# Optimization experiments

Hardware: AMD Instinct MI355X
Metric: run time of the kernel (lower is better)

The kernel has to match this reference:

```python
import jax, jax.numpy as jnp
import numpy as np

B, N, DV = 32, 1024, 512
L, S, DT = 256, 8, 512
VOCAB = 1024
BAND = 16
LN_EPS = 1e-5


def setup_inputs() -> dict:
    key = jax.random.key(0)
    ks = jax.random.split(key, 12)
    w = lambda k, shp: jax.random.normal(k, shp, dtype=jnp.float32) * 0.02
    return {
        "vis_tokens": jax.random.normal(ks[0], (B, N, DV), dtype=jnp.float32),
        "txt_ctx_ids": jax.random.randint(ks[1], (B, L, S), 0, VOCAB, dtype=jnp.int32),
        "emb_w": w(ks[2], (VOCAB, DT)),        # embedding table, tied with classifier
        "wq": w(ks[3], (DV, DT)),              # q_proj: d_txt -> d_vis
        "wk": w(ks[4], (DV, DV)),
        "wv": w(ks[5], (DV, DV)),
        "wv2t": w(ks[6], (DT, DV)),            # vis2txt: d_vis -> d_txt
        "dw_k": w(ks[7], (DT, 1, 3)),          # depthwise conv1d kernel (O, I/g=1, K)
        "pw_k": w(ks[8], (DT, DT, 1)),         # pointwise conv1d kernel
        "ln_g": jnp.ones((DT,), jnp.float32),
        "ln_b": jnp.zeros((DT,), jnp.float32),
        "dir_alpha": jnp.float32(0.2),
    }


def reference(vis_tokens, txt_ctx_ids, emb_w, wq, wk, wv, wv2t, dw_k, pw_k, ln_g, ln_b, dir_alpha):
    b, n, dv = vis_tokens.shape
    E = emb_w[txt_ctx_ids]                       # [B, L, S, Dt]
    bl = b * E.shape[1]
    x = E.reshape(bl, E.shape[2], DT).transpose(0, 2, 1)  # [B*L, Dt, S]
    dn = ('NCH', 'OIH', 'NCH')
    h = jax.lax.conv_general_dilated(x, dw_k, (1,), 'SAME', dimension_numbers=dn,
                                     feature_group_count=DT)
    y = jax.lax.conv_general_dilated(jax.nn.silu(h), pw_k, (1,), 'SAME', dimension_numbers=dn)
    x = x + y
    m = x.mean(axis=2)                           # [B*L, Dt]
    mu = m.mean(-1, keepdims=True)
    var = ((m - mu) ** 2).mean(-1, keepdims=True)
    q_txt = ((m - mu) * jax.lax.rsqrt(var + LN_EPS) * ln_g + ln_b).reshape(b, -1, DT)  # [B, L, Dt]

    Q = q_txt @ wq.T                             # [B, L, Dv]
    K = vis_tokens @ wk.T                        # [B, N, Dv]
    V = vis_tokens @ wv.T
    logits = jnp.einsum('bld,bnd->bln', Q, K) * (dv ** -0.5)

    # linear centers (torch linspace(0, N-1, L).long() truncates toward zero)
    centers = jnp.linspace(0.0, n - 1, q_txt.shape[1]).astype(jnp.int32)  # [L]
    centers = jnp.broadcast_to(centers[None, :], (b, q_txt.shape[1]))
    idx = jnp.arange(n)[None, None, :]
    signed = (centers[..., None] - idx).astype(jnp.float32)
    logits = logits + dir_alpha * (signed / (BAND + 1e-6))
    keep = jnp.abs(idx - centers[..., None]) <= BAND
    logits = jnp.where(keep, logits, -jnp.inf)

    A = jax.nn.softmax(logits, axis=-1)          # [B, L, N]
    Fv = jnp.einsum('bln,bnd->bld', A, V)        # dropout in source is undefined attr; identity
    H = Fv @ wv2t.T                              # [B, L, Dt]
    cls = H @ emb_w.T                            # tied classifier
    return (cls, H, A)
```

## Files before the change

### kernel.cpp

```cpp
#include <hip/hip_runtime.h>
#include <cmath>

typedef unsigned short u16;
typedef __attribute__((ext_vector_type(8))) short bf16x8;
typedef __attribute__((ext_vector_type(4))) float f32x4;
typedef __attribute__((ext_vector_type(8))) unsigned short u16x8;

#define B_  32
#define N_  1024
#define L_  256
#define S_  8
#define DT_ 512
#define BAND_ 16

__device__ __forceinline__ u16 f2bf(float f) {
  union { float f; unsigned u; } x; x.f = f;
  unsigned r = (x.u + 0x7fffu + ((x.u >> 16) & 1u)) >> 16;
  return (u16)r;
}
__device__ __forceinline__ float bf2f(u16 h) {
  union { unsigned u; float f; } x; x.u = ((unsigned)h) << 16;
  return x.f;
}

#define B1_WAIT(N)                                       \
  asm volatile("s_waitcnt vmcnt(" #N ")" ::: "memory");  \
  __builtin_amdgcn_s_barrier();                          \
  __builtin_amdgcn_sched_barrier(0);
#define B2_BAR()                                         \
  __builtin_amdgcn_sched_barrier(0);                     \
  __builtin_amdgcn_s_barrier();

__global__ __launch_bounds__(256) void cvt_bf16(
    const float* __restrict__ in, u16* __restrict__ out, int n4) {
  int i = blockIdx.x * 256 + threadIdx.x;
  if (i < n4) {
    float4 v = ((const float4*)in)[i];
    ushort4 o;
    o.x = f2bf(v.x); o.y = f2bf(v.y); o.z = f2bf(v.z); o.w = f2bf(v.w);
    ((ushort4*)out)[i] = o;
  }
}

__global__ __launch_bounds__(256) void cvt_weights(
    const float* __restrict__ e, const float* __restrict__ q,
    const float* __restrict__ k, const float* __restrict__ v,
    const float* __restrict__ t, const float* __restrict__ pw,
    u16* __restrict__ eo, u16* __restrict__ qo, u16* __restrict__ kvo,
    u16* __restrict__ to, u16* __restrict__ po) {
  int i = blockIdx.x * 256 + threadIdx.x;
  const float* src; u16* dst; int soff, doff;
  if (i < 131072)      { src = e;  dst = eo;  soff = i;          doff = soff; }
  else if (i < 196608) { src = q;  dst = qo;  soff = i - 131072; doff = soff; }
  else if (i < 262144) { src = k;  dst = kvo; soff = i - 196608; doff = soff; }
  else if (i < 327680) { src = v;  dst = kvo; soff = i - 262144; doff = soff + 65536; }
  else if (i < 393216) { src = t;  dst = to;  soff = i - 327680; doff = soff; }
  else                 { src = pw; dst = po;  soff = i - 393216; doff = soff; }
  float4 vv = ((const float4*)src)[soff];
  ushort4 o;
  o.x = f2bf(vv.x); o.y = f2bf(vv.y); o.z = f2bf(vv.z); o.w = f2bf(vv.w);
  ((ushort4*)dst)[doff] = o;
}

__global__ __launch_bounds__(256) void text_front(
    const int* __restrict__ ids, const float* __restrict__ emb,
    const float* __restrict__ dwk, u16* __restrict__ shm,
    float* __restrict__ mbuf) {
  int bl = blockIdx.x;
  int tid = threadIdx.x;
  __shared__ int sid[S_];
  if (tid < S_) sid[tid] = ids[bl * S_ + tid];
  __syncthreads();
  for (int c = tid; c < DT_; c += 256) {
    float x[S_];
#pragma unroll
    for (int s = 0; s < S_; ++s) x[s] = emb[(size_t)sid[s] * DT_ + c];
    float k0 = dwk[c * 3 + 0], k1 = dwk[c * 3 + 1], k2 = dwk[c * 3 + 2];
    float me = 0.f, sh = 0.f;
#pragma unroll
    for (int s = 0; s < S_; ++s) {
      float xm = (s > 0) ? x[s - 1] : 0.0f;
      float xp = (s < S_ - 1) ? x[s + 1] : 0.0f;
      float h = k0 * xm + k1 * x[s] + k2 * xp;
      float si = h / (1.0f + expf(-h));
      me += x[s];
      sh += si;
    }
    shm[(size_t)bl * DT_ + c] = f2bf(sh * (1.0f / S_));
    mbuf[(size_t)bl * DT_ + c] = me * (1.0f / S_);
  }
}

__global__ __launch_bounds__(512) void gemm_kv_8ph(
    const u16* __restrict__ A, const u16* __restrict__ B,
    u16* __restrict__ Cb, int M, int N, int K) {
  __shared__ u16 As[32768];
  __shared__ u16 Bs[32768];
  const int tid = threadIdx.x;
  const int w = tid >> 6;
  const int lane = tid & 63;
  const int wm = w >> 2, wn = w & 3;

  const int gx = gridDim.x;
  const int bid = blockIdx.y * gx + blockIdx.x;
  const int nwg = gx * gridDim.y;
  const int logical = (bid & 7) * (nwg >> 3) + (bid >> 3);
  const int bm = (logical / gx) << 8;
  const int bn = (logical % gx) << 8;

  const int rowS0 = (w << 5) + (lane >> 2);
  const int rowS1 = rowS0 + 16;
  const int gac = (((lane & 3) ^ ((lane >> 3) & 3)) << 3);
  const u16* AgS0 = A + (size_t)(bm + rowS0) * K + gac;
  const u16* AgS1 = A + (size_t)(bm + rowS1) * K + gac;
  const u16* BgS0 = B + (size_t)(bn + rowS0) * K + gac;
  const u16* BgS1 = B + (size_t)(bn + rowS1) * K + gac;
  const int ldsS0 = (w << 10) + 0;
  const int ldsS1 = (w << 10) + 512;

#define STAGE(step)                                                           \
  {                                                                           \
    const int bufo_ = ((step) & 3) << 13;                                     \
    const int ks_ = (step) << 5;                                              \
    __builtin_amdgcn_global_load_lds(                                         \
        (const __attribute__((address_space(1))) void*)(AgS0 + ks_),          \
        (__attribute__((address_space(3))) void*)(As + bufo_ + ldsS0), 16, 0, 0); \
    __builtin_amdgcn_global_load_lds(                                         \
        (const __attribute__((address_space(1))) void*)(AgS1 + ks_),          \
        (__attribute__((address_space(3))) void*)(As + bufo_ + ldsS1), 16, 0, 0); \
    __builtin_amdgcn_global_load_lds(                                         \
        (const __attribute__((address_space(1))) void*)(BgS0 + ks_),          \
        (__attribute__((address_space(3))) void*)(Bs + bufo_ + ldsS0), 16, 0, 0); \
    __builtin_amdgcn_global_load_lds(                                         \
        (const __attribute__((address_space(1))) void*)(BgS1 + ks_),          \
        (__attribute__((address_space(3))) void*)(Bs + bufo_ + ldsS1), 16, 0, 0); \
  }

  const int kg = lane >> 4;
  int aoff[8], boff[4];
#pragma unroll
  for (int m = 0; m < 8; ++m) {
    const int r = (wm << 7) + (m << 4) + (lane & 15);
    aoff[m] = (r << 5) + ((kg ^ ((r >> 1) & 3)) << 3);
  }
#pragma unroll
  for (int n = 0; n < 4; ++n) {
    const int r = (wn << 6) + (n << 4) + (lane & 15);
    boff[n] = (r << 5) + ((kg ^ ((r >> 1) & 3)) << 3);
  }

  f32x4 acc[8][4];
#pragma unroll
  for (int m = 0; m < 8; ++m)
#pragma unroll
    for (int n = 0; n < 4; ++n) acc[m][n] = (f32x4){0.f, 0.f, 0.f, 0.f};

#define GROUP_BODY(sbuf)                                                      \
  {                                                                           \
    const u16* Ab = As + ((sbuf) << 13);                                      \
    const u16* Bb = Bs + ((sbuf) << 13);                                      \
    bf16x8 af[8], bfr[4];                                                     \
    _Pragma("unroll")                                                         \
    for (int m = 0; m < 8; ++m) af[m] = *(const bf16x8*)(Ab + aoff[m]);       \
    _Pragma("unroll")                                                         \
    for (int n = 0; n < 4; ++n) bfr[n] = *(const bf16x8*)(Bb + boff[n]);      \
    asm volatile("s_waitcnt lgkmcnt(0)" ::: "memory");                        \
    __builtin_amdgcn_sched_barrier(0);                                        \
    __builtin_amdgcn_s_setprio(1);                                            \
    _Pragma("unroll")                                                         \
    for (int m = 0; m < 8; ++m)                                               \
      _Pragma("unroll")                                                       \
      for (int n = 0; n < 4; ++n)                                             \
        acc[m][n] = __builtin_amdgcn_mfma_f32_16x16x32_bf16(                  \
            af[m], bfr[n], acc[m][n], 0, 0, 0);                               \
    __builtin_amdgcn_s_setprio(0);                                            \
  }

  const int nt = K >> 5;
  STAGE(0)
  STAGE(1)
  STAGE(2)
  for (int s = 0; s <= nt - 4; ++s) {
    __builtin_amdgcn_s_barrier();
    STAGE(s + 3)
    B1_WAIT(12)
    GROUP_BODY(s & 3)
  }
  __builtin_amdgcn_s_barrier();
  B1_WAIT(8)
  GROUP_BODY((nt - 3) & 3)
  __builtin_amdgcn_s_barrier();
  B1_WAIT(4)
  GROUP_BODY((nt - 2) & 3)
  __builtin_amdgcn_s_barrier();
  B1_WAIT(0)
  GROUP_BODY((nt - 1) & 3)
#undef GROUP_BODY
#undef STAGE

  const int rb = bm + (wm << 7) + ((lane >> 4) << 2);
  const int cb = bn + (wn << 6) + (lane & 15);
#pragma unroll
  for (int m = 0; m < 8; ++m)
#pragma unroll
    for (int n = 0; n < 4; ++n) {
      const int col = cb + (n << 4);
#pragma unroll
      for (int j = 0; j < 4; ++j) {
        size_t idx = (size_t)(rb + (m << 4) + j) * N + col;
        Cb[idx] = f2bf(acc[m][n][j]);
      }
    }
}

template <bool ACC, bool WF32, bool WBF16>
__global__ __launch_bounds__(256) void gemm_mfma(
    const u16* __restrict__ A, const u16* __restrict__ B,
    float* __restrict__ C, u16* __restrict__ Cb, int M, int N, int K) {
  __shared__ u16 As[8192];
  __shared__ u16 Bs[8192];
  const int tid = threadIdx.x;
  const int w = tid >> 6;
  const int lane = tid & 63;

  const int gx = gridDim.x;
  const int bid = blockIdx.y * gx + blockIdx.x;
  const int nwg = gx * gridDim.y;
  const int logical = (bid & 7) * (nwg >> 3) + (bid >> 3);
  const int bm = (logical / gx) << 7;
  const int bn = (logical % gx) << 7;
  const int wr = w >> 1, wc = w & 1;

  const int r0 = (w << 4) + (lane >> 2);
  const int kc = (lane & 3) << 3;
  const u16* Ag0 = A + (size_t)(bm + r0) * K + kc;
  const u16* Ag1 = Ag0 + (size_t)64 * K;
  const u16* Bg0 = B + (size_t)(bn + r0) * K + kc;
  const u16* Bg1 = Bg0 + (size_t)64 * K;

  int aoff[4], boff[4];
#pragma unroll
  for (int m = 0; m < 4; ++m)
    aoff[m] = (((wr << 6) + (m << 4) + (lane & 15)) << 5) + ((lane >> 4) << 3);
#pragma unroll
  for (int n = 0; n < 4; ++n)
    boff[n] = (((wc << 6) + (n << 4) + (lane & 15)) << 5) + ((lane >> 4) << 3);

  f32x4 acc[4][4];
#pragma unroll
  for (int m = 0; m < 4; ++m)
#pragma unroll
    for (int n = 0; n < 4; ++n) acc[m][n] = (f32x4){0.f, 0.f, 0.f, 0.f};

#define STAGE(buf, kt)                                                        \
  {                                                                           \
    u16* as_ = As + (buf) * 4096 + (w << 9);                                  \
    u16* bs_ = Bs + (buf) * 4096 + (w << 9);                                  \
    __builtin_amdgcn_global_load_lds(                                         \
        (const __attribute__((address_space(1))) void*)(Ag0 + (kt)),          \
        (__attribute__((address_space(3))) void*)as_, 16, 0, 0);              \
    __builtin_amdgcn_global_load_lds(                                         \
        (const __attribute__((address_space(1))) void*)(Ag1 + (kt)),          \
        (__attribute__((address_space(3))) void*)(as_ + 2048), 16, 0, 0);     \
    __builtin_amdgcn_global_load_lds(                                         \
        (const __attribute__((address_space(1))) void*)(Bg0 + (kt)),          \
        (__attribute__((address_space(3))) void*)bs_, 16, 0, 0);              \
    __builtin_amdgcn_global_load_lds(                                         \
        (const __attribute__((address_space(1))) void*)(Bg1 + (kt)),          \
        (__attribute__((address_space(3))) void*)(bs_ + 2048), 16, 0, 0);     \
  }

  const int nt = K >> 5;
  STAGE(0, 0);
  int cur = 0;
  for (int t = 0; t < nt; ++t) {
    if (t + 1 < nt) {
      STAGE(cur ^ 1, (t + 1) << 5);
      B1_WAIT(4)
    } else {
      B1_WAIT(0)
    }
    const u16* Ab = As + cur * 4096;
    const u16* Bb = Bs + cur * 4096;
    bf16x8 af[4], bfr[4];
#pragma unroll
    for (int m = 0; m < 4; ++m) af[m] = *(const bf16x8*)(Ab + aoff[m]);
#pragma unroll
    for (int n = 0; n < 4; ++n) bfr[n] = *(const bf16x8*)(Bb + boff[n]);
#pragma unroll
    for (int m = 0; m < 4; ++m)
#pragma unroll
      for (int n = 0; n < 4; ++n)
        acc[m][n] = __builtin_amdgcn_mfma_f32_16x16x32_bf16(
            af[m], bfr[n], acc[m][n], 0, 0, 0);
    B2_BAR()
    cur ^= 1;
  }
#undef STAGE

  const int rb = bm + (wr << 6) + ((lane >> 4) << 2);
  const int cb = bn + (wc << 6) + (lane & 15);
#pragma unroll
  for (int m = 0; m < 4; ++m)
#pragma unroll
    for (int n = 0; n < 4; ++n) {
      int col = cb + (n << 4);
#pragma unroll
      for (int j = 0; j < 4; ++j) {
        size_t idx = (size_t)(rb + (m << 4) + j) * N + col;
        float v = acc[m][n][j];
        if (ACC) v += C[idx];
        if (WF32) C[idx] = v;
        if (WBF16) Cb[idx] = f2bf(v);
      }
    }
}

template <bool ACC, bool WF32, bool WBF16>
__global__ __launch_bounds__(256) void gemm_n64(
    const u16* __restrict__ A, const u16* __restrict__ B,
    float* __restrict__ C, u16* __restrict__ Cb, int M, int N, int K) {
  __shared__ u16 As[8192];
  __shared__ u16 Bs[4096];
  const int tid = threadIdx.x;
  const int w = tid >> 6;
  const int lane = tid & 63;

  const int gx = gridDim.x;
  const int bid = blockIdx.y * gx + blockIdx.x;
  const int nwg = gx * gridDim.y;
  const int logical = (bid & 7) * (nwg >> 3) + (bid >> 3);
  const int bm = (logical / gx) << 7;
  const int bn = (logical % gx) << 6;

  const int r0 = (w << 4) + (lane >> 2);
  const int kc = (lane & 3) << 3;
  const u16* Ag0 = A + (size_t)(bm + r0) * K + kc;
  const u16* Ag1 = Ag0 + (size_t)64 * K;
  const u16* Bg0 = B + (size_t)(bn + r0) * K + kc;

  int aoff[2], boff[4];
#pragma unroll
  for (int m = 0; m < 2; ++m)
    aoff[m] = (((w << 5) + (m << 4) + (lane & 15)) << 5) + ((lane >> 4) << 3);
#pragma unroll
  for (int n = 0; n < 4; ++n)
    boff[n] = (((n << 4) + (lane & 15)) << 5) + ((lane >> 4) << 3);

  f32x4 acc[2][4];
#pragma unroll
  for (int m = 0; m < 2; ++m)
#pragma unroll
    for (int n = 0; n < 4; ++n) acc[m][n] = (f32x4){0.f, 0.f, 0.f, 0.f};

#define STAGE(buf, kt)                                                        \
  {                                                                           \
    u16* as_ = As + (buf) * 4096 + (w << 9);                                  \
    u16* bs_ = Bs + (buf) * 2048 + (w << 9);                                  \
    __builtin_amdgcn_global_load_lds(                                         \
        (const __attribute__((address_space(1))) void*)(Ag0 + (kt)),          \
        (__attribute__((address_space(3))) void*)as_, 16, 0, 0);              \
    __builtin_amdgcn_global_load_lds(                                         \
        (const __attribute__((address_space(1))) void*)(Ag1 + (kt)),          \
        (__attribute__((address_space(3))) void*)(as_ + 2048), 16, 0, 0);     \
    __builtin_amdgcn_global_load_lds(                                         \
        (const __attribute__((address_space(1))) void*)(Bg0 + (kt)),          \
        (__attribute__((address_space(3))) void*)bs_, 16, 0, 0);              \
  }

  const int nt = K >> 5;
  STAGE(0, 0);
  int cur = 0;
  for (int t = 0; t < nt; ++t) {
    if (t + 1 < nt) {
      STAGE(cur ^ 1, (t + 1) << 5);
      B1_WAIT(3)
    } else {
      B1_WAIT(0)
    }
    const u16* Ab = As + cur * 4096;
    const u16* Bb = Bs + cur * 2048;
    bf16x8 af[2], bfr[4];
#pragma unroll
    for (int m = 0; m < 2; ++m) af[m] = *(const bf16x8*)(Ab + aoff[m]);
#pragma unroll
    for (int n = 0; n < 4; ++n) bfr[n] = *(const bf16x8*)(Bb + boff[n]);
#pragma unroll
    for (int m = 0; m < 2; ++m)
#pragma unroll
      for (int n = 0; n < 4; ++n)
        acc[m][n] = __builtin_amdgcn_mfma_f32_16x16x32_bf16(
            af[m], bfr[n], acc[m][n], 0, 0, 0);
    B2_BAR()
    cur ^= 1;
  }
#undef STAGE

  const int rb = bm + (w << 5) + ((lane >> 4) << 2);
  const int cb = bn + (lane & 15);
#pragma unroll
  for (int m = 0; m < 2; ++m)
#pragma unroll
    for (int n = 0; n < 4; ++n) {
      int col = cb + (n << 4);
#pragma unroll
      for (int j = 0; j < 4; ++j) {
        size_t idx = (size_t)(rb + (m << 4) + j) * N + col;
        float v = acc[m][n][j];
        if (ACC) v += C[idx];
        if (WF32) C[idx] = v;
        if (WBF16) Cb[idx] = f2bf(v);
      }
    }
}

__global__ __launch_bounds__(256) void ln_kernel(
    const float* __restrict__ m, const float* __restrict__ g,
    const float* __restrict__ bta, u16* __restrict__ q) {
  int row = blockIdx.x;
  int tid = threadIdx.x;
  float v0 = m[(size_t)row * 512 + tid];
  float v1 = m[(size_t)row * 512 + 256 + tid];
  __shared__ float red[4], red2[4];
  float s = v0 + v1;
#pragma unroll
  for (int d = 32; d; d >>= 1) s += __shfl_xor(s, d);
  if ((tid & 63) == 0) red[tid >> 6] = s;
  __syncthreads();
  float mu = (red[0] + red[1] + red[2] + red[3]) * (1.0f / 512.0f);
  float d0 = v0 - mu, d1 = v1 - mu;
  float s2 = d0 * d0 + d1 * d1;
#pragma unroll
  for (int d = 32; d; d >>= 1) s2 += __shfl_xor(s2, d);
  if ((tid & 63) == 0) red2[tid >> 6] = s2;
  __syncthreads();
  float var = (red2[0] + red2[1] + red2[2] + red2[3]) * (1.0f / 512.0f);
  float r = rsqrtf(var + 1e-5f);
  q[(size_t)row * 512 + tid] = f2bf(d0 * r * g[tid] + bta[tid]);
  q[(size_t)row * 512 + 256 + tid] = f2bf(d1 * r * g[tid + 256] + bta[tid + 256]);
}

__global__ __launch_bounds__(512) void attn_kernel(
    const u16* __restrict__ Qb, const u16* __restrict__ KV,
    const float* __restrict__ alpha_p, float* __restrict__ A,
    u16* __restrict__ Fv) {
  __shared__ u16 KV_s[96 * 512];
  __shared__ u16 Q_s[16 * 520];
  __shared__ float S_s[16 * 100];

  const int bid = blockIdx.x;
  const int logical = (bid & 7) * 64 + (bid >> 3);
  const int b = logical >> 4, lg = logical & 15;
  const int l0 = lg * 16;
  const int tid = threadIdx.x;
  const int w = tid >> 6, lane = tid & 63;
  const float al = *alpha_p;

  const int c_min = (1023 * l0) / 255;
  const int kb0 = min(max(c_min - BAND_, 0), N_ - 96);

  {
    const size_t rowb = (size_t)(b * N_ + kb0);
    for (int rr = 0; rr < 12; ++rr) {
      const int r = w * 12 + rr;
      const u16* src = KV + (rowb + r) * 1024 + ((lane * 8) ^ ((r & 7) << 3));
      u16* dst = KV_s + r * 512;
      __builtin_amdgcn_global_load_lds(
          (const __attribute__((address_space(1))) void*)src,
          (__attribute__((address_space(3))) void*)dst, 16, 0, 0);
    }
  }
  {
    const int r = tid >> 5;
    const u16* qrow = Qb + (size_t)(b * L_ + l0 + r) * 512;
#pragma unroll
    for (int h = 0; h < 2; ++h) {
      const int ch = (tid & 31) + h * 32;
      u16x8 v = *(const u16x8*)(qrow + ch * 8);
      *(u16x8*)(Q_s + r * 520 + ch * 8) = v;
    }
  }
  __syncthreads();

  if (w < 6) {
    f32x4 acc = {0.f, 0.f, 0.f, 0.f};
    const int arow = (lane & 15) * 520 + ((lane >> 4) << 3);
    const int key = w * 16 + (lane & 15);
    const int swz = (key & 7) << 3;
    for (int ks = 0; ks < 16; ++ks) {
      bf16x8 aq = *(const bf16x8*)(Q_s + arow + ks * 32);
      bf16x8 bk =
          *(const bf16x8*)(KV_s + key * 512 + ((ks * 32 + ((lane >> 4) << 3)) ^ swz));
      acc = __builtin_amdgcn_mfma_f32_16x16x32_bf16(aq, bk, acc, 0, 0, 0);
    }
#pragma unroll
    for (int j = 0; j < 4; ++j)
      S_s[((lane >> 4) * 4 + j) * 100 + w * 16 + (lane & 15)] = acc[j];
  }
  __syncthreads();

  {
    const size_t rowb = (size_t)(b * N_ + kb0);
    for (int rr = 0; rr < 12; ++rr) {
      const int r = w * 12 + rr;
      const u16* src =
          KV + (rowb + r) * 1024 + 512 + ((lane * 8) ^ ((r & 7) << 3));
      u16* dst = KV_s + r * 512;
      __builtin_amdgcn_global_load_lds(
          (const __attribute__((address_space(1))) void*)src,
          (__attribute__((address_space(3))) void*)dst, 16, 0, 0);
    }
  }

#pragma unroll
  for (int rr = 0; rr < 2; ++rr) {
    const int l = 2 * w + rr;
    const int c = (1023 * (l0 + l)) / 255;
    const int g0 = kb0 + lane, g1 = kb0 + 64 + lane;
    const bool v0 = (g0 >= c - BAND_) && (g0 <= c + BAND_);
    const bool v1 = (lane < 32) && (g1 >= c - BAND_) && (g1 <= c + BAND_);
    const float sc = 0.044194173824159216f;
    float x0 = v0 ? S_s[l * 100 + lane] * sc +
                        al * ((float)(c - g0) * (1.0f / 16.000001f))
                  : -INFINITY;
    float x1 = v1 ? S_s[l * 100 + 64 + lane] * sc +
                        al * ((float)(c - g1) * (1.0f / 16.000001f))
                  : -INFINITY;
    float mx = fmaxf(x0, x1);
#pragma unroll
    for (int d = 32; d; d >>= 1) mx = fmaxf(mx, __shfl_xor(mx, d));
    float e0 = v0 ? expf(x0 - mx) : 0.0f;
    float e1 = v1 ? expf(x1 - mx) : 0.0f;
    float sm = e0 + e1;
#pragma unroll
    for (int d = 32; d; d >>= 1) sm += __shfl_xor(sm, d);
    const float inv = 1.0f / sm;
    S_s[l * 100 + lane] = e0 * inv;
    if (lane < 32) S_s[l * 100 + 64 + lane] = e1 * inv;
    const int lo = max(0, c - BAND_), hi = min(N_ - 1, c + BAND_);
    float* Arow = A + (size_t)(b * L_ + l0 + l) * N_;
#pragma unroll
    for (int p4 = 0; p4 < 4; ++p4) {
      const int p = (p4 * 64 + lane) * 4;
      float4 v;
      v.x = (p + 0 >= lo && p + 0 <= hi) ? S_s[l * 100 + p + 0 - kb0] : 0.0f;
      v.y = (p + 1 >= lo && p + 1 <= hi) ? S_s[l * 100 + p + 1 - kb0] : 0.0f;
      v.z = (p + 2 >= lo && p + 2 <= hi) ? S_s[l * 100 + p + 2 - kb0] : 0.0f;
      v.w = (p + 3 >= lo && p + 3 <= hi) ? S_s[l * 100 + p + 3 - kb0] : 0.0f;
      ((float4*)Arow)[p4 * 64 + lane] = v;
    }
  }
  __syncthreads();

#pragma unroll
  for (int rr = 0; rr < 2; ++rr) {
    const int l = 2 * w + rr;
    const int c = (1023 * (l0 + l)) / 255;
    const int jlo = max(0, c - BAND_) - kb0, jhi = min(N_ - 1, c + BAND_) - kb0;
    float acc[8] = {};
    for (int j = jlo; j <= jhi; ++j) {
      const float avj = S_s[l * 100 + j];
      const u16x8 v =
          *(const u16x8*)(KV_s + j * 512 + ((lane * 8) ^ ((j & 7) << 3)));
#pragma unroll
      for (int t = 0; t < 8; ++t) acc[t] += avj * bf2f(v[t]);
    }
    u16x8 fo;
#pragma unroll
    for (int t = 0; t < 8; ++t) fo[t] = f2bf(acc[t]);
    *(u16x8*)(Fv + (size_t)(b * L_ + l0 + l) * 512 + lane * 8) = fo;
  }
}

extern "C" void kernel_launch(void* const* d_in, const int* in_sizes, int n_in,
                              void* d_out, int out_size, void* d_ws,
                              size_t ws_size, hipStream_t stream) {
  const float* vis = (const float*)d_in[0];
  const int* ids = (const int*)d_in[1];
  const float* emb = (const float*)d_in[2];
  const float* wq = (const float*)d_in[3];
  const float* wk = (const float*)d_in[4];
  const float* wvp = (const float*)d_in[5];
  const float* wv2t = (const float*)d_in[6];
  const float* dwk = (const float*)d_in[7];
  const float* pwk = (const float*)d_in[8];
  const float* lng = (const float*)d_in[9];
  const float* lnb = (const float*)d_in[10];
  const float* alpha = (const float*)d_in[11];

  float* out_cls = (float*)d_out;
  float* out_H = out_cls + (size_t)8192 * 1024;
  float* out_A = out_H + (size_t)8192 * 512;

  char* p = (char*)d_ws;
  u16* visb = (u16*)p;              p += (size_t)32768 * 512 * 2;
  u16* KVb  = (u16*)p;              p += (size_t)32768 * 1024 * 2;
  u16* embb = (u16*)p;              p += (size_t)1024 * 512 * 2;
  u16* wqb  = (u16*)p;              p += (size_t)512 * 512 * 2;
  u16* wkvb = (u16*)p;              p += (size_t)1024 * 512 * 2;
  u16* wv2tb= (u16*)p;              p += (size_t)512 * 512 * 2;
  u16* pwkb = (u16*)p;              p += (size_t)512 * 512 * 2;
  u16* shmb = (u16*)p;              p += (size_t)8192 * 512 * 2;
  float* mbuf = (float*)p;          p += (size_t)8192 * 512 * 4;
  u16* qbuf = (u16*)p;              p += (size_t)8192 * 512 * 2;
  u16* Qbf  = (u16*)p;              p += (size_t)8192 * 512 * 2;
  u16* Fvb  = (u16*)p;              p += (size_t)8192 * 512 * 2;
  u16* Hb   = (u16*)p;              p += (size_t)8192 * 512 * 2;

  cvt_bf16<<<16384, 256, 0, stream>>>(vis, visb, 32768 * 512 / 4);
  cvt_weights<<<1792, 256, 0, stream>>>(emb, wq, wk, wvp, wv2t, pwk,
                                        embb, wqb, wkvb, wv2tb, pwkb);

  gemm_kv_8ph<<<dim3(4, 128), 512, 0, stream>>>(
      visb, wkvb, KVb, 32768, 1024, 512);

  text_front<<<8192, 256, 0, stream>>>(ids, emb, dwk, shmb, mbuf);
  gemm_n64<true, true, false><<<dim3(8, 64), 256, 0, stream>>>(
      shmb, pwkb, mbuf, nullptr, 8192, 512, 512);
  ln_kernel<<<8192, 256, 0, stream>>>(mbuf, lng, lnb, qbuf);
  gemm_n64<false, false, true><<<dim3(8, 64), 256, 0, stream>>>(
      qbuf, wqb, nullptr, Qbf, 8192, 512, 512);
  attn_kernel<<<512, 512, 0, stream>>>(Qbf, KVb, alpha, out_A, Fvb);
  gemm_n64<false, true, true><<<dim3(8, 64), 256, 0, stream>>>(
      Fvb, wv2tb, out_H, Hb, 8192, 512, 512);
  gemm_mfma<false, true, false><<<dim3(8, 64), 256, 0, stream>>>(
      Hb, embb, out_cls, nullptr, 8192, 1024, 512);
}
```

Before: 211.8 us.

## Fuse fp32-to-bf16 conversion of visual tokens into the KV GEMM A-load

Drops the separate cvt_bf16 pass over vis_tokens. The KV GEMM now reads the fp32 activations directly into registers, packs them to bf16 with v_cvt_pk_bf16_f32, and writes them into swizzled LDS, in a register-staged software pipeline alongside the async B loads. This removes a full write and re-read of a 32 MB bf16 intermediate plus one kernel launch. In exchange the GEMM reads fp32 (twice the A bytes, re-read by each of 4 column blocks), adds VGPR pressure, and hardcodes the K-loop trip count for K=512.

```diff
diff --git a/kernel.cpp b/kernel.cpp
--- a/kernel.cpp
+++ b/kernel.cpp
@@ -21,6 +21,11 @@
 __device__ __forceinline__ float bf2f(u16 h) {
   union { unsigned u; float f; } x; x.u = ((unsigned)h) << 16;
   return x.f;
+}
+__device__ __forceinline__ unsigned cvtpk(float lo, float hi) {
+  unsigned r;
+  asm volatile("v_cvt_pk_bf16_f32 %0, %1, %2" : "=v"(r) : "v"(lo), "v"(hi));
+  return r;
 }
 
 #define B1_WAIT(N)                                       \
@@ -30,17 +35,6 @@
 #define B2_BAR()                                         \
   __builtin_amdgcn_sched_barrier(0);                     \
   __builtin_amdgcn_s_barrier();
-
-__global__ __launch_bounds__(256) void cvt_bf16(
-    const float* __restrict__ in, u16* __restrict__ out, int n4) {
-  int i = blockIdx.x * 256 + threadIdx.x;
-  if (i < n4) {
-    float4 v = ((const float4*)in)[i];
-    ushort4 o;
-    o.x = f2bf(v.x); o.y = f2bf(v.y); o.z = f2bf(v.z); o.w = f2bf(v.w);
-    ((ushort4*)out)[i] = o;
-  }
-}
 
 __global__ __launch_bounds__(256) void cvt_weights(
     const float* __restrict__ e, const float* __restrict__ q,
@@ -92,7 +86,7 @@
 }
 
 __global__ __launch_bounds__(512) void gemm_kv_8ph(
-    const u16* __restrict__ A, const u16* __restrict__ B,
+    const float* __restrict__ A, const u16* __restrict__ B,
     u16* __restrict__ Cb, int M, int N, int K) {
   __shared__ u16 As[32768];
   __shared__ u16 Bs[32768];
@@ -108,26 +102,47 @@
   const int bm = (logical / gx) << 8;
   const int bn = (logical % gx) << 8;
 
+  const int arow = tid >> 1;
+  const float* Ap = A + (size_t)(bm + arow) * K + ((tid & 1) << 4);
+  const int ac0 = (tid & 1) << 1;
+  const int aswz = (arow >> 1) & 3;
+  const int woff0 = (arow << 5) + (((ac0 + 0) ^ aswz) << 3);
+  const int woff1 = (arow << 5) + (((ac0 + 1) ^ aswz) << 3);
+
   const int rowS0 = (w << 5) + (lane >> 2);
   const int rowS1 = rowS0 + 16;
   const int gac = (((lane & 3) ^ ((lane >> 3) & 3)) << 3);
-  const u16* AgS0 = A + (size_t)(bm + rowS0) * K + gac;
-  const u16* AgS1 = A + (size_t)(bm + rowS1) * K + gac;
   const u16* BgS0 = B + (size_t)(bn + rowS0) * K + gac;
   const u16* BgS1 = B + (size_t)(bn + rowS1) * K + gac;
   const int ldsS0 = (w << 10) + 0;
   const int ldsS1 = (w << 10) + 512;
 
-#define STAGE(step)                                                           \
+  float4 sreg[2][4];
+
+#define LOADA(P, step)                                        \
+  sreg[P][0] = *(const float4*)(Ap + ((step) << 5));          \
+  sreg[P][1] = *(const float4*)(Ap + ((step) << 5) + 4);      \
+  sreg[P][2] = *(const float4*)(Ap + ((step) << 5) + 8);      \
+  sreg[P][3] = *(const float4*)(Ap + ((step) << 5) + 12);
+#define WRITEA(P, step)                                       \
+  {                                                           \
+    uint4 q0, q1;                                             \
+    q0.x = cvtpk(sreg[P][0].x, sreg[P][0].y);                 \
+    q0.y = cvtpk(sreg[P][0].z, sreg[P][0].w);                 \
+    q0.z = cvtpk(sreg[P][1].x, sreg[P][1].y);                 \
+    q0.w = cvtpk(sreg[P][1].z, sreg[P][1].w);                 \
+    q1.x = cvtpk(sreg[P][2].x, sreg[P][2].y);                 \
+    q1.y = cvtpk(sreg[P][2].z, sreg[P][2].w);                 \
+    q1.z = cvtpk(sreg[P][3].x, sreg[P][3].y);                 \
+    q1.w = cvtpk(sreg[P][3].z, sreg[P][3].w);                 \
+    u16* ab = As + (((step) & 3) << 13);                      \
+    *(uint4*)(ab + woff0) = q0;                               \
+    *(uint4*)(ab + woff1) = q1;                               \
+  }
+#define STAGEB(step)                                                          \
   {                                                                           \
     const int bufo_ = ((step) & 3) << 13;                                     \
     const int ks_ = (step) << 5;                                              \
-    __builtin_amdgcn_global_load_lds(                                         \
-        (const __attribute__((address_space(1))) void*)(AgS0 + ks_),          \
-        (__attribute__((address_space(3))) void*)(As + bufo_ + ldsS0), 16, 0, 0); \
-    __builtin_amdgcn_global_load_lds(                                         \
-        (const __attribute__((address_space(1))) void*)(AgS1 + ks_),          \
-        (__attribute__((address_space(3))) void*)(As + bufo_ + ldsS1), 16, 0, 0); \
     __builtin_amdgcn_global_load_lds(                                         \
         (const __attribute__((address_space(1))) void*)(BgS0 + ks_),          \
         (__attribute__((address_space(3))) void*)(Bs + bufo_ + ldsS0), 16, 0, 0); \
@@ -176,27 +191,40 @@
     __builtin_amdgcn_s_setprio(0);                                            \
   }
 
-  const int nt = K >> 5;
-  STAGE(0)
-  STAGE(1)
-  STAGE(2)
-  for (int s = 0; s <= nt - 4; ++s) {
+  LOADA(0, 0)
+  STAGEB(0)
+  LOADA(1, 1)
+  STAGEB(1)
+  asm volatile("s_waitcnt vmcnt(2)" ::: "memory");
+  __builtin_amdgcn_sched_barrier(0);
+  WRITEA(0, 0)
+  WRITEA(1, 1)
+  LOADA(0, 2)
+  STAGEB(2)
+  asm volatile("s_waitcnt lgkmcnt(0)" ::: "memory");
+
+  for (int s = 0; s <= 12; ++s) {
     __builtin_amdgcn_s_barrier();
-    STAGE(s + 3)
-    B1_WAIT(12)
+    LOADA((s + 3) & 1, s + 3)
+    STAGEB(s + 3)
+    B1_WAIT(8)
+    WRITEA((s + 2) & 1, s + 2)
     GROUP_BODY(s & 3)
   }
   __builtin_amdgcn_s_barrier();
-  B1_WAIT(8)
-  GROUP_BODY((nt - 3) & 3)
+  B1_WAIT(2)
+  WRITEA(1, 15)
+  GROUP_BODY(1)
   __builtin_amdgcn_s_barrier();
-  B1_WAIT(4)
-  GROUP_BODY((nt - 2) & 3)
+  B1_WAIT(2)
+  GROUP_BODY(2)
   __builtin_amdgcn_s_barrier();
   B1_WAIT(0)
-  GROUP_BODY((nt - 1) & 3)
+  GROUP_BODY(3)
 #undef GROUP_BODY
-#undef STAGE
+#undef STAGEB
+#undef WRITEA
+#undef LOADA
 
   const int rb = bm + (wm << 7) + ((lane >> 4) << 2);
   const int cb = bn + (wn << 6) + (lane & 15);
@@ -593,7 +621,6 @@
   float* out_A = out_H + (size_t)8192 * 512;
 
   char* p = (char*)d_ws;
-  u16* visb = (u16*)p;              p += (size_t)32768 * 512 * 2;
   u16* KVb  = (u16*)p;              p += (size_t)32768 * 1024 * 2;
   u16* embb = (u16*)p;              p += (size_t)1024 * 512 * 2;
   u16* wqb  = (u16*)p;              p += (size_t)512 * 512 * 2;
@@ -607,12 +634,11 @@
   u16* Fvb  = (u16*)p;              p += (size_t)8192 * 512 * 2;
   u16* Hb   = (u16*)p;              p += (size_t)8192 * 512 * 2;
 
-  cvt_bf16<<<16384, 256, 0, stream>>>(vis, visb, 32768 * 512 / 4);
   cvt_weights<<<1792, 256, 0, stream>>>(emb, wq, wk, wvp, wv2t, pwk,
                                         embb, wqb, wkvb, wv2tb, pwkb);
 
   gemm_kv_8ph<<<dim3(4, 128), 512, 0, stream>>>(
-      visb, wkvb, KVb, 32768, 1024, 512);
+      vis, wkvb, KVb, 32768, 1024, 512);
 
   text_front<<<8192, 256, 0, stream>>>(ids, emb, dwk, shmb, mbuf);
   gemm_n64<true, true, false><<<dim3(8, 64), 256, 0, stream>>>(
```

Result: no change. 212.9 us (+0.5%).
